# Performance work log

Measured on AMD Instinct MI355X. Metric: run time of the kernel, lower is better.

The kernel has to match this reference:

```python
import jax, jax.numpy as jnp
import numpy as np

N_NODES = 50000
N_EDGES = 800000
D_FEAT = 128
N_LAYERS = 3
HALF = 64  # units // 2 per kernel in tf_geometric MeanGraphSage
HIDDEN = 256
NUM_LABELS = 40


def setup_inputs() -> dict:
    key = jax.random.key(0)
    ks = jax.random.split(key, 6)
    x = jax.random.normal(ks[0], (N_NODES, D_FEAT), dtype=jnp.float32)
    edge_index = jax.random.randint(ks[1], (2, N_EDGES), 0, N_NODES, dtype=jnp.int32)
    self_kernels = jax.random.normal(ks[2], (N_LAYERS, D_FEAT, HALF), dtype=jnp.float32) * 0.05
    neighbor_kernels = jax.random.normal(ks[3], (N_LAYERS, D_FEAT, HALF), dtype=jnp.float32) * 0.05
    biases = jnp.zeros((N_LAYERS, 2 * HALF), dtype=jnp.float32)
    mlp_w1 = jax.random.normal(ks[4], (2 * HALF, HIDDEN), dtype=jnp.float32) * 0.05
    mlp_b1 = jnp.zeros((HIDDEN,), dtype=jnp.float32)
    mlp_w2 = jax.random.normal(ks[5], (HIDDEN, NUM_LABELS), dtype=jnp.float32) * 0.05
    mlp_b2 = jnp.zeros((NUM_LABELS,), dtype=jnp.float32)
    return {"x": x, "edge_index": edge_index, "self_kernels": self_kernels,
            "neighbor_kernels": neighbor_kernels, "biases": biases,
            "mlp_w1": mlp_w1, "mlp_b1": mlp_b1, "mlp_w2": mlp_w2, "mlp_b2": mlp_b2}


def reference(x, edge_index, self_kernels, neighbor_kernels, biases,
              mlp_w1, mlp_b1, mlp_w2, mlp_b2):
    n = x.shape[0]
    row, col = edge_index[0], edge_index[1]  # row: target node, col: source node
    # in-degree counts (graph is fixed across layers)
    ones = jnp.ones((edge_index.shape[1],), dtype=x.dtype)
    deg = jax.ops.segment_sum(ones, row, num_segments=n)  # [N]
    inv_deg = (1.0 / jnp.maximum(deg, 1.0))[:, None]      # [N,1]

    h = x
    for i in range(N_LAYERS):
        # mean-neighbor aggregation: gather source feats, segment-sum to targets
        nbr_sum = jax.ops.segment_sum(h[col], row, num_segments=n)  # [N,D]
        nbr_mean = nbr_sum * inv_deg
        from_self = h @ self_kernels[i]        # [N,HALF]
        from_nbr = nbr_mean @ neighbor_kernels[i]  # [N,HALF]
        h = jax.nn.relu(jnp.concatenate([from_self, from_nbr], axis=1) + biases[i])

    # MLP head (Flatten on [N,128] is a no-op)
    h = jax.nn.relu(h @ mlp_w1 + mlp_b1)
    return h @ mlp_w2 + mlp_b2
```

## Files before the change

kernel.cpp:

```cpp
#include <hip/hip_runtime.h>
#include <hip/hip_bf16.h>
#include <cstdint>
#include <cstddef>

#define N_NODES 50000
#define N_PAD   50176
#define N_EDGES 800000
#define D_FEAT  128
#define HALF    64
#define HIDDEN  256
#define LABELS  40

#define NBUCK 196
#define BCAP  5632
#define EDGES_PER_BLK 4096

#define HID_STRIDE 264

typedef __attribute__((ext_vector_type(8))) short bf16x8;
typedef __attribute__((ext_vector_type(4))) float f32x4;

#define PK_SELF(L) ((size_t)(L) * 8192)
#define PK_NBR(L)  (24576 + (size_t)(L) * 8192)
#define PK_W1      49152
#define PK_W2      81920
#define PK_TOTAL   94208

__device__ inline uint16_t f2bf_bits(float f) {
    __hip_bfloat16 b = __float2bfloat16(f);
    uint16_t u; __builtin_memcpy(&u, &b, 2); return u;
}

__global__ __launch_bounds__(1024) void bucket_scatter_kernel(
        const int* __restrict__ row, const int* __restrict__ col,
        int* __restrict__ bucket_cursor, uint32_t* __restrict__ staged) {
    __shared__ int hist[NBUCK];
    __shared__ int hbase[NBUCK];
    int tid  = threadIdx.x;
    int e0   = blockIdx.x * EDGES_PER_BLK;
    int eend = e0 + EDGES_PER_BLK; if (eend > N_EDGES) eend = N_EDGES;

    for (int i = tid; i < NBUCK; i += 1024) hist[i] = 0;
    __syncthreads();

    int rr[4], cc[4]; int ne = 0;
    for (int e = e0 + tid; e < eend; e += 1024) {
        rr[ne] = row[e]; cc[ne] = col[e]; ne++;
    }
    for (int i = 0; i < ne; i++) atomicAdd(&hist[rr[i] >> 8], 1);
    __syncthreads();

    for (int i = tid; i < NBUCK; i += 1024) {
        hbase[i] = atomicAdd(&bucket_cursor[i], hist[i]);
        hist[i]  = 0;
    }
    __syncthreads();

    for (int i = 0; i < ne; i++) {
        int b   = rr[i] >> 8;
        int off = atomicAdd(&hist[b], 1);
        int pos = hbase[b] + off;
        if (pos < BCAP)
            staged[(size_t)b * BCAP + pos] =
                ((uint32_t)(rr[i] & 255) << 16) | (uint32_t)cc[i];
    }
}

__global__ __launch_bounds__(1024) void bucket_fill_kernel(
        const uint32_t* __restrict__ staged, const int* __restrict__ bucket_cursor,
        int* __restrict__ deg, int* __restrict__ rowstart,
        float* __restrict__ inv_deg, int* __restrict__ csr_col) {
    __shared__ int cnt[256];
    __shared__ int excl[256];
    __shared__ int wt[4];
    __shared__ int seg[BCAP];
    __shared__ int base_s;
    int b   = blockIdx.x;
    int tid = threadIdx.x;

    if (tid < 64) {
        int partial = 0;
        for (int i = tid; i < b; i += 64) partial += bucket_cursor[i];
#pragma unroll
        for (int off = 32; off > 0; off >>= 1)
            partial += __shfl_down(partial, off, 64);
        if (tid == 0) base_s = partial;
    }
    if (tid < 256) cnt[tid] = 0;
    __syncthreads();

    int total = bucket_cursor[b]; if (total > BCAP) total = BCAP;
    int gbase = base_s;
    const uint32_t* st = staged + (size_t)b * BCAP;

    for (int i = tid; i < total; i += 1024) atomicAdd(&cnt[st[i] >> 16], 1);
    __syncthreads();

    int lane = tid & 63, wid = tid >> 6;
    int v = 0, s = 0;
    if (tid < 256) {
        v = cnt[tid]; s = v;
#pragma unroll
        for (int off = 1; off < 64; off <<= 1) {
            int t = __shfl_up(s, off, 64);
            if (lane >= off) s += t;
        }
        if (lane == 63) wt[wid] = s;
    }
    __syncthreads();
    if (tid == 0) { int a = 0; for (int i = 0; i < 4; i++) { int t = wt[i]; wt[i] = a; a += t; } }
    __syncthreads();
    if (tid < 256) {
        int ex = s - v + wt[wid];
        excl[tid] = ex;
        int node = (b << 8) + tid;
        if (node < N_NODES) {
            deg[node]      = v;
            rowstart[node] = gbase + ex;
            inv_deg[node]  = 1.0f / fmaxf((float)v, 1.0f);
        }
    }
    __syncthreads();
    for (int i = tid; i < total; i += 1024) {
        uint32_t u = st[i];
        int p = atomicAdd(&excl[u >> 16], 1);
        seg[p] = (int)(u & 0xffffu);
    }
    __syncthreads();
    for (int i = tid; i < total; i += 1024) csr_col[gbase + i] = seg[i];
}

__global__ __launch_bounds__(256) void xcast_kernel(
        const float* __restrict__ x, __hip_bfloat16* __restrict__ xb) {
    size_t i = (size_t)(blockIdx.x * blockDim.x + threadIdx.x) * 4;
    if (i >= (size_t)N_NODES * D_FEAT) return;
    float4 v = *(const float4*)(x + i);
    uint2 p;
    p.x = (uint32_t)f2bf_bits(v.x) | ((uint32_t)f2bf_bits(v.y) << 16);
    p.y = (uint32_t)f2bf_bits(v.z) | ((uint32_t)f2bf_bits(v.w) << 16);
    *(uint2*)((uint16_t*)xb + i) = p;
}

__global__ __launch_bounds__(256) void pack_all_kernel(
        const float* __restrict__ selfk, const float* __restrict__ nbrk,
        const float* __restrict__ w1, const float* __restrict__ w2,
        __hip_bfloat16* __restrict__ wpack) {
    int m = blockIdx.y;
    const float* W; int K, Ncols, Npad; size_t dstoff;
    if (m < 3)      { W = selfk + (size_t)m*D_FEAT*HALF;      K=128; Ncols=64;  Npad=64;  dstoff = PK_SELF(m); }
    else if (m < 6) { W = nbrk  + (size_t)(m-3)*D_FEAT*HALF;  K=128; Ncols=64;  Npad=64;  dstoff = PK_NBR(m-3); }
    else if (m == 6){ W = w1;                                 K=128; Ncols=256; Npad=256; dstoff = PK_W1; }
    else            { W = w2;                                 K=256; Ncols=40;  Npad=48;  dstoff = PK_W2; }
    int ksteps = K / 32;
    int total  = ksteps * (Npad / 16) * 64;
    int t = blockIdx.x * blockDim.x + threadIdx.x;
    if (t >= total) return;
    int lane = t & 63;
    int rest = t >> 6;
    int ks   = rest % ksteps;
    int ns   = rest / ksteps;
    int colb = ns * 16 + (lane & 15);
    int kb   = ks * 32 + (lane >> 4) * 8;
    __hip_bfloat16* dst = wpack + dstoff + (size_t)t * 8;
#pragma unroll
    for (int j = 0; j < 8; j++) {
        float v = (colb < Ncols) ? W[(size_t)(kb + j) * Ncols + colb] : 0.f;
        dst[j] = __float2bfloat16(v);
    }
}

__global__ __launch_bounds__(256) void agg4_kernel(
        const __hip_bfloat16* __restrict__ h, const int* __restrict__ csr_col,
        const int* __restrict__ rowstart, const int* __restrict__ deg,
        const float* __restrict__ inv_deg, __hip_bfloat16* __restrict__ nbr) {
    int gid  = blockIdx.x * blockDim.x + threadIdx.x;
    int wnum = gid >> 6;
    int lane = threadIdx.x & 63;
    int sub  = lane >> 4;
    int sl   = lane & 15;
    int node = wnum * 4 + sub;
    int start = rowstart[node];
    int d     = deg[node];
    const uint32_t* hw = (const uint32_t*)h;
    float acc[8] = {};

#define ACC8(U)                                        \
    acc[0] += __uint_as_float((U).x << 16);            \
    acc[1] += __uint_as_float((U).x & 0xffff0000u);    \
    acc[2] += __uint_as_float((U).y << 16);            \
    acc[3] += __uint_as_float((U).y & 0xffff0000u);    \
    acc[4] += __uint_as_float((U).z << 16);            \
    acc[5] += __uint_as_float((U).z & 0xffff0000u);    \
    acc[6] += __uint_as_float((U).w << 16);            \
    acc[7] += __uint_as_float((U).w & 0xffff0000u);

    if (d > 0) {
        int last = start + d - 1;
        int s[8];
#pragma unroll
        for (int k = 0; k < 8; k++) s[k] = csr_col[min(start + k, last)];
        int j = 0;
        for (; j + 8 <= d; j += 8) {
            int p[8];
#pragma unroll
            for (int k = 0; k < 8; k++) p[k] = csr_col[min(start + j + 8 + k, last)];
            uint4 u0 = *(const uint4*)(hw + (size_t)s[0] * 64 + sl * 4);
            uint4 u1 = *(const uint4*)(hw + (size_t)s[1] * 64 + sl * 4);
            uint4 u2 = *(const uint4*)(hw + (size_t)s[2] * 64 + sl * 4);
            uint4 u3 = *(const uint4*)(hw + (size_t)s[3] * 64 + sl * 4);
            uint4 u4 = *(const uint4*)(hw + (size_t)s[4] * 64 + sl * 4);
            uint4 u5 = *(const uint4*)(hw + (size_t)s[5] * 64 + sl * 4);
            uint4 u6 = *(const uint4*)(hw + (size_t)s[6] * 64 + sl * 4);
            uint4 u7 = *(const uint4*)(hw + (size_t)s[7] * 64 + sl * 4);
            ACC8(u0); ACC8(u1); ACC8(u2); ACC8(u3);
            ACC8(u4); ACC8(u5); ACC8(u6); ACC8(u7);
#pragma unroll
            for (int k = 0; k < 8; k++) s[k] = p[k];
        }
        int r = d - j;
#pragma unroll
        for (int k = 0; k < 8; k++) {
            if (k < r) {
                uint4 u = *(const uint4*)(hw + (size_t)s[k] * 64 + sl * 4);
                ACC8(u);
            }
        }
    }
#undef ACC8

    float inv = inv_deg[node];
    uint4 p;
    p.x = (uint32_t)f2bf_bits(acc[0] * inv) | ((uint32_t)f2bf_bits(acc[1] * inv) << 16);
    p.y = (uint32_t)f2bf_bits(acc[2] * inv) | ((uint32_t)f2bf_bits(acc[3] * inv) << 16);
    p.z = (uint32_t)f2bf_bits(acc[4] * inv) | ((uint32_t)f2bf_bits(acc[5] * inv) << 16);
    p.w = (uint32_t)f2bf_bits(acc[6] * inv) | ((uint32_t)f2bf_bits(acc[7] * inv) << 16);
    *(uint4*)((uint32_t*)nbr + (size_t)node * 64 + sl * 4) = p;
}

__global__ __launch_bounds__(256, 2) void layer_fused_kernel(
        const __hip_bfloat16* __restrict__ h, const __hip_bfloat16* __restrict__ nbr,
        const __hip_bfloat16* __restrict__ wpack_self,
        const __hip_bfloat16* __restrict__ wpack_nbr,
        const float* __restrict__ bias, __hip_bfloat16* __restrict__ out) {
    int wave = threadIdx.x >> 6, lane = threadIdx.x & 63;
    int row0 = blockIdx.x * 128 + wave * 32;
    int lrow = lane & 15, lgrp = lane >> 4;
    const __hip_bfloat16* hr0 = h   + (size_t)(row0 + lrow) * D_FEAT + lgrp * 8;
    const __hip_bfloat16* hr1 = hr0 + (size_t)16 * D_FEAT;
    const __hip_bfloat16* nr0 = nbr + (size_t)(row0 + lrow) * D_FEAT + lgrp * 8;
    const __hip_bfloat16* nr1 = nr0 + (size_t)16 * D_FEAT;

    f32x4 accS[2][4] = {};
    f32x4 accN[2][4] = {};
#pragma unroll
    for (int ks = 0; ks < 4; ks++) {
        bf16x8 ah0 = *(const bf16x8*)(hr0 + ks * 32);
        bf16x8 ah1 = *(const bf16x8*)(hr1 + ks * 32);
        bf16x8 an0 = *(const bf16x8*)(nr0 + ks * 32);
        bf16x8 an1 = *(const bf16x8*)(nr1 + ks * 32);
#pragma unroll
        for (int ns = 0; ns < 4; ns++) {
            bf16x8 bs = *(const bf16x8*)(wpack_self + ((size_t)(ns * 4 + ks) * 64 + lane) * 8);
            accS[0][ns] = __builtin_amdgcn_mfma_f32_16x16x32_bf16(ah0, bs, accS[0][ns], 0, 0, 0);
            accS[1][ns] = __builtin_amdgcn_mfma_f32_16x16x32_bf16(ah1, bs, accS[1][ns], 0, 0, 0);
            bf16x8 bn = *(const bf16x8*)(wpack_nbr + ((size_t)(ns * 4 + ks) * 64 + lane) * 8);
            accN[0][ns] = __builtin_amdgcn_mfma_f32_16x16x32_bf16(an0, bn, accN[0][ns], 0, 0, 0);
            accN[1][ns] = __builtin_amdgcn_mfma_f32_16x16x32_bf16(an1, bn, accN[1][ns], 0, 0, 0);
        }
    }
#pragma unroll
    for (int t = 0; t < 2; t++) {
#pragma unroll
        for (int ns = 0; ns < 4; ns++) {
            int colS = ns * 16 + lrow;
            int colN = HALF + colS;
            float bvS = bias[colS];
            float bvN = bias[colN];
#pragma unroll
            for (int i = 0; i < 4; i++) {
                int r = row0 + t * 16 + lgrp * 4 + i;
                out[(size_t)r * D_FEAT + colS] =
                    __float2bfloat16(fmaxf(accS[t][ns][i] + bvS, 0.f));
                out[(size_t)r * D_FEAT + colN] =
                    __float2bfloat16(fmaxf(accN[t][ns][i] + bvN, 0.f));
            }
        }
    }
}

__global__ __launch_bounds__(256, 2) void mlp_fused_kernel(
        const __hip_bfloat16* __restrict__ h, const __hip_bfloat16* __restrict__ w1p,
        const float* __restrict__ b1, const __hip_bfloat16* __restrict__ w2p,
        const float* __restrict__ b2, float* __restrict__ out) {
    __shared__ __align__(16) uint16_t hid[128 * HID_STRIDE];
    int wave = threadIdx.x >> 6, lane = threadIdx.x & 63;
    int row0 = blockIdx.x * 128 + wave * 32;
    int lrow = lane & 15, lgrp = lane >> 4;

    {
        const __hip_bfloat16* ar0 = h + (size_t)(row0 + lrow) * D_FEAT + lgrp * 8;
        const __hip_bfloat16* ar1 = ar0 + (size_t)16 * D_FEAT;
        f32x4 acc[2][16] = {};
#pragma unroll 1
        for (int ks = 0; ks < 4; ks++) {
            bf16x8 a0 = *(const bf16x8*)(ar0 + ks * 32);
            bf16x8 a1 = *(const bf16x8*)(ar1 + ks * 32);
#pragma unroll
            for (int ns = 0; ns < 16; ns++) {
                bf16x8 bfr = *(const bf16x8*)(w1p + ((size_t)(ns * 4 + ks) * 64 + lane) * 8);
                acc[0][ns] = __builtin_amdgcn_mfma_f32_16x16x32_bf16(a0, bfr, acc[0][ns], 0, 0, 0);
                acc[1][ns] = __builtin_amdgcn_mfma_f32_16x16x32_bf16(a1, bfr, acc[1][ns], 0, 0, 0);
            }
        }
        int lbase = wave * 32;
#pragma unroll
        for (int t = 0; t < 2; t++) {
#pragma unroll
            for (int ns = 0; ns < 16; ns++) {
                int col = ns * 16 + lrow;
                float bv = b1[col];
#pragma unroll
                for (int i = 0; i < 4; i++) {
                    int lr = lbase + t * 16 + lgrp * 4 + i;
                    hid[lr * HID_STRIDE + col] =
                        f2bf_bits(fmaxf(acc[t][ns][i] + bv, 0.f));
                }
            }
        }
    }
    __syncthreads();

    const uint16_t* br0 = &hid[(wave * 32 + lrow) * HID_STRIDE + lgrp * 8];
    const uint16_t* br1 = br0 + 16 * HID_STRIDE;
    f32x4 acc2[2][3] = {};
#pragma unroll
    for (int ks = 0; ks < 8; ks++) {
        bf16x8 a0 = *(const bf16x8*)(br0 + ks * 32);
        bf16x8 a1 = *(const bf16x8*)(br1 + ks * 32);
#pragma unroll
        for (int ns = 0; ns < 3; ns++) {
            bf16x8 bfr = *(const bf16x8*)(w2p + ((size_t)(ns * 8 + ks) * 64 + lane) * 8);
            acc2[0][ns] = __builtin_amdgcn_mfma_f32_16x16x32_bf16(a0, bfr, acc2[0][ns], 0, 0, 0);
            acc2[1][ns] = __builtin_amdgcn_mfma_f32_16x16x32_bf16(a1, bfr, acc2[1][ns], 0, 0, 0);
        }
    }
#pragma unroll
    for (int t = 0; t < 2; t++) {
#pragma unroll
        for (int ns = 0; ns < 3; ns++) {
            int col = ns * 16 + lrow;
            if (col < LABELS) {
                float bv = b2[col];
#pragma unroll
                for (int i = 0; i < 4; i++) {
                    int r = row0 + t * 16 + lgrp * 4 + i;
                    if (r < N_NODES)
                        out[(size_t)r * LABELS + col] = acc2[t][ns][i] + bv;
                }
            }
        }
    }
}

extern "C" void kernel_launch(void* const* d_in, const int* in_sizes, int n_in,
                              void* d_out, int out_size, void* d_ws, size_t ws_size,
                              hipStream_t stream) {
    const float* x      = (const float*)d_in[0];
    const int*   ei     = (const int*)d_in[1];
    const float* selfk  = (const float*)d_in[2];
    const float* nbrk   = (const float*)d_in[3];
    const float* biases = (const float*)d_in[4];
    const float* w1     = (const float*)d_in[5];
    const float* b1     = (const float*)d_in[6];
    const float* w2     = (const float*)d_in[7];
    const float* b2     = (const float*)d_in[8];
    float* out = (float*)d_out;

    const int* row = ei;
    const int* col = ei + N_EDGES;

    char* ws = (char*)d_ws;
    size_t off = 0;
    auto alloc = [&](size_t bytes) -> char* {
        char* p = ws + off;
        off = (off + bytes + 255) & ~(size_t)255;
        return p;
    };
    int*   deg       = (int*)  alloc((size_t)N_NODES * 4);
    int*   rowstart  = (int*)  alloc((size_t)N_NODES * 4);
    float* inv_deg   = (float*)alloc((size_t)N_NODES * 4);
    int*   bucket_cursor = (int*)alloc(256 * 4);
    int*   csr_col   = (int*)  alloc((size_t)N_EDGES * 4);
    uint32_t* staged = (uint32_t*)alloc((size_t)NBUCK * BCAP * 4);
    __hip_bfloat16* wpack  = (__hip_bfloat16*)alloc(PK_TOTAL * 2);
    __hip_bfloat16* xb     = (__hip_bfloat16*)alloc((size_t)N_PAD * D_FEAT * 2);
    __hip_bfloat16* hA     = (__hip_bfloat16*)alloc((size_t)N_PAD * D_FEAT * 2);
    __hip_bfloat16* hB     = (__hip_bfloat16*)alloc((size_t)N_PAD * D_FEAT * 2);
    __hip_bfloat16* nbrbuf = (__hip_bfloat16*)alloc((size_t)N_PAD * D_FEAT * 2);

    hipMemsetAsync(bucket_cursor, 0, 256 * 4, stream);

    const int scat_blocks = (N_EDGES + EDGES_PER_BLK - 1) / EDGES_PER_BLK;
    bucket_scatter_kernel<<<scat_blocks, 1024, 0, stream>>>(row, col, bucket_cursor, staged);
    bucket_fill_kernel<<<NBUCK, 1024, 0, stream>>>(staged, bucket_cursor,
                                                   deg, rowstart, inv_deg, csr_col);

    xcast_kernel<<<(N_NODES * D_FEAT / 4 + 255) / 256, 256, 0, stream>>>(x, xb);
    dim3 pgrid(16, 8);
    pack_all_kernel<<<pgrid, 256, 0, stream>>>(selfk, nbrk, w1, w2, wpack);

    const int agg_blocks   = N_NODES / 16;
    const int layer_blocks = N_PAD / 128;
    const int mlp_blocks   = N_PAD / 128;

    const __hip_bfloat16* hcur = xb;
    __hip_bfloat16* bufs[3] = {hA, hB, hA};
    for (int L = 0; L < 3; L++) {
        agg4_kernel<<<agg_blocks, 256, 0, stream>>>(hcur, csr_col, rowstart, deg,
                                                    inv_deg, nbrbuf);
        layer_fused_kernel<<<layer_blocks, 256, 0, stream>>>(
            hcur, nbrbuf, wpack + PK_SELF(L), wpack + PK_NBR(L),
            biases + (size_t)L * (2 * HALF), bufs[L]);
        hcur = bufs[L];
    }

    mlp_fused_kernel<<<mlp_blocks, 256, 0, stream>>>(hcur, wpack + PK_W1, b1,
                                                     wpack + PK_W2, b2, out);
}
```

Baseline: 247.4 us.

## Store node features in 16-column panels to localize gathers per panel

Reorganizes all bf16 feature buffers into 8 panels of 16 features each and splits the neighbor aggregation across panels, so each block gathers 32-byte slices from a single panel. This aims to keep the working set of the random gather small enough to stay cache-resident rather than streaming full 256-byte rows. The layer and MLP kernels are adapted to read and write the panel layout. The cost is re-reading the CSR indices and degree data once per panel and issuing more, smaller loads.

```diff
diff --git a/kernel.cpp b/kernel.cpp
--- a/kernel.cpp
+++ b/kernel.cpp
@@ -16,6 +16,8 @@
 #define EDGES_PER_BLK 4096
 
 #define HID_STRIDE 264
+
+#define PANE ((size_t)N_PAD * 16)
 
 typedef __attribute__((ext_vector_type(8))) short bf16x8;
 typedef __attribute__((ext_vector_type(4))) float f32x4;
@@ -130,15 +132,24 @@
     for (int i = tid; i < total; i += 1024) csr_col[gbase + i] = seg[i];
 }
 
-__global__ __launch_bounds__(256) void xcast_kernel(
-        const float* __restrict__ x, __hip_bfloat16* __restrict__ xb) {
-    size_t i = (size_t)(blockIdx.x * blockDim.x + threadIdx.x) * 4;
-    if (i >= (size_t)N_NODES * D_FEAT) return;
-    float4 v = *(const float4*)(x + i);
-    uint2 p;
-    p.x = (uint32_t)f2bf_bits(v.x) | ((uint32_t)f2bf_bits(v.y) << 16);
-    p.y = (uint32_t)f2bf_bits(v.z) | ((uint32_t)f2bf_bits(v.w) << 16);
-    *(uint2*)((uint16_t*)xb + i) = p;
+__global__ __launch_bounds__(256) void xcast_panel_kernel(
+        const float* __restrict__ x, __hip_bfloat16* __restrict__ hP) {
+    int idx = blockIdx.x * blockDim.x + threadIdx.x;
+    if (idx >= 8 * N_NODES * 2) return;
+    int p    = idx / (N_NODES * 2);
+    int rem  = idx - p * (N_NODES * 2);
+    int node = rem >> 1;
+    int half = rem & 1;
+    const float* src = x + (size_t)node * D_FEAT + p * 16 + half * 8;
+    float4 v0 = *(const float4*)src;
+    float4 v1 = *(const float4*)(src + 4);
+    uint2 o0, o1;
+    o0.x = (uint32_t)f2bf_bits(v0.x) | ((uint32_t)f2bf_bits(v0.y) << 16);
+    o0.y = (uint32_t)f2bf_bits(v0.z) | ((uint32_t)f2bf_bits(v0.w) << 16);
+    o1.x = (uint32_t)f2bf_bits(v1.x) | ((uint32_t)f2bf_bits(v1.y) << 16);
+    o1.y = (uint32_t)f2bf_bits(v1.z) | ((uint32_t)f2bf_bits(v1.w) << 16);
+    uint32_t* dst = (uint32_t*)(hP + (size_t)p * PANE + (size_t)node * 16 + half * 8);
+    dst[0] = o0.x; dst[1] = o0.y; dst[2] = o1.x; dst[3] = o1.y;
 }
 
 __global__ __launch_bounds__(256) void pack_all_kernel(
@@ -169,30 +180,28 @@
     }
 }
 
-__global__ __launch_bounds__(256) void agg4_kernel(
-        const __hip_bfloat16* __restrict__ h, const int* __restrict__ csr_col,
+__global__ __launch_bounds__(256) void agg_panel_kernel(
+        const __hip_bfloat16* __restrict__ hP, const int* __restrict__ csr_col,
         const int* __restrict__ rowstart, const int* __restrict__ deg,
-        const float* __restrict__ inv_deg, __hip_bfloat16* __restrict__ nbr) {
-    int gid  = blockIdx.x * blockDim.x + threadIdx.x;
-    int wnum = gid >> 6;
-    int lane = threadIdx.x & 63;
-    int sub  = lane >> 4;
-    int sl   = lane & 15;
-    int node = wnum * 4 + sub;
-    int start = rowstart[node];
-    int d     = deg[node];
-    const uint32_t* hw = (const uint32_t*)h;
-    float acc[8] = {};
-
-#define ACC8(U)                                        \
+        const float* __restrict__ inv_deg, __hip_bfloat16* __restrict__ nbrP) {
+    int panel = blockIdx.x & 7;
+    int chunk = blockIdx.x >> 3;
+    int wave  = threadIdx.x >> 6;
+    int lane  = threadIdx.x & 63;
+    int sub   = lane >> 2;
+    int q     = lane & 3;
+    int node  = (chunk * 4 + wave) * 16 + sub;
+    int ne    = min(node, N_NODES - 1);
+    int start = rowstart[ne];
+    int d     = deg[ne];
+    const uint32_t* hw = (const uint32_t*)(hP + (size_t)panel * PANE);
+    float acc[4] = {};
+
+#define ACC4(U)                                        \
     acc[0] += __uint_as_float((U).x << 16);            \
     acc[1] += __uint_as_float((U).x & 0xffff0000u);    \
     acc[2] += __uint_as_float((U).y << 16);            \
-    acc[3] += __uint_as_float((U).y & 0xffff0000u);    \
-    acc[4] += __uint_as_float((U).z << 16);            \
-    acc[5] += __uint_as_float((U).z & 0xffff0000u);    \
-    acc[6] += __uint_as_float((U).w << 16);            \
-    acc[7] += __uint_as_float((U).w & 0xffff0000u);
+    acc[3] += __uint_as_float((U).y & 0xffff0000u);
 
     if (d > 0) {
         int last = start + d - 1;
@@ -204,16 +213,16 @@
             int p[8];
 #pragma unroll
             for (int k = 0; k < 8; k++) p[k] = csr_col[min(start + j + 8 + k, last)];
-            uint4 u0 = *(const uint4*)(hw + (size_t)s[0] * 64 + sl * 4);
-            uint4 u1 = *(const uint4*)(hw + (size_t)s[1] * 64 + sl * 4);
-            uint4 u2 = *(const uint4*)(hw + (size_t)s[2] * 64 + sl * 4);
-            uint4 u3 = *(const uint4*)(hw + (size_t)s[3] * 64 + sl * 4);
-            uint4 u4 = *(const uint4*)(hw + (size_t)s[4] * 64 + sl * 4);
-            uint4 u5 = *(const uint4*)(hw + (size_t)s[5] * 64 + sl * 4);
-            uint4 u6 = *(const uint4*)(hw + (size_t)s[6] * 64 + sl * 4);
-            uint4 u7 = *(const uint4*)(hw + (size_t)s[7] * 64 + sl * 4);
-            ACC8(u0); ACC8(u1); ACC8(u2); ACC8(u3);
-            ACC8(u4); ACC8(u5); ACC8(u6); ACC8(u7);
+            uint2 u0 = *(const uint2*)(hw + (size_t)s[0] * 8 + q * 2);
+            uint2 u1 = *(const uint2*)(hw + (size_t)s[1] * 8 + q * 2);
+            uint2 u2 = *(const uint2*)(hw + (size_t)s[2] * 8 + q * 2);
+            uint2 u3 = *(const uint2*)(hw + (size_t)s[3] * 8 + q * 2);
+            uint2 u4 = *(const uint2*)(hw + (size_t)s[4] * 8 + q * 2);
+            uint2 u5 = *(const uint2*)(hw + (size_t)s[5] * 8 + q * 2);
+            uint2 u6 = *(const uint2*)(hw + (size_t)s[6] * 8 + q * 2);
+            uint2 u7 = *(const uint2*)(hw + (size_t)s[7] * 8 + q * 2);
+            ACC4(u0); ACC4(u1); ACC4(u2); ACC4(u3);
+            ACC4(u4); ACC4(u5); ACC4(u6); ACC4(u7);
 #pragma unroll
             for (int k = 0; k < 8; k++) s[k] = p[k];
         }
@@ -221,20 +230,18 @@
 #pragma unroll
         for (int k = 0; k < 8; k++) {
             if (k < r) {
-                uint4 u = *(const uint4*)(hw + (size_t)s[k] * 64 + sl * 4);
-                ACC8(u);
+                uint2 u = *(const uint2*)(hw + (size_t)s[k] * 8 + q * 2);
+                ACC4(u);
             }
         }
     }
-#undef ACC8
-
-    float inv = inv_deg[node];
-    uint4 p;
+#undef ACC4
+
+    float inv = inv_deg[ne];
+    uint2 p;
     p.x = (uint32_t)f2bf_bits(acc[0] * inv) | ((uint32_t)f2bf_bits(acc[1] * inv) << 16);
     p.y = (uint32_t)f2bf_bits(acc[2] * inv) | ((uint32_t)f2bf_bits(acc[3] * inv) << 16);
-    p.z = (uint32_t)f2bf_bits(acc[4] * inv) | ((uint32_t)f2bf_bits(acc[5] * inv) << 16);
-    p.w = (uint32_t)f2bf_bits(acc[6] * inv) | ((uint32_t)f2bf_bits(acc[7] * inv) << 16);
-    *(uint4*)((uint32_t*)nbr + (size_t)node * 64 + sl * 4) = p;
+    *(uint2*)((uint32_t*)(nbrP + (size_t)panel * PANE) + (size_t)node * 8 + q * 2) = p;
 }
 
 __global__ __launch_bounds__(256, 2) void layer_fused_kernel(
@@ -245,19 +252,19 @@
     int wave = threadIdx.x >> 6, lane = threadIdx.x & 63;
     int row0 = blockIdx.x * 128 + wave * 32;
     int lrow = lane & 15, lgrp = lane >> 4;
-    const __hip_bfloat16* hr0 = h   + (size_t)(row0 + lrow) * D_FEAT + lgrp * 8;
-    const __hip_bfloat16* hr1 = hr0 + (size_t)16 * D_FEAT;
-    const __hip_bfloat16* nr0 = nbr + (size_t)(row0 + lrow) * D_FEAT + lgrp * 8;
-    const __hip_bfloat16* nr1 = nr0 + (size_t)16 * D_FEAT;
+    size_t psel = (size_t)(lgrp >> 1) * PANE;
+    size_t rb0  = (size_t)(row0 + lrow) * 16 + (lgrp & 1) * 8;
+    size_t rb1  = rb0 + 16 * 16;
 
     f32x4 accS[2][4] = {};
     f32x4 accN[2][4] = {};
 #pragma unroll
     for (int ks = 0; ks < 4; ks++) {
-        bf16x8 ah0 = *(const bf16x8*)(hr0 + ks * 32);
-        bf16x8 ah1 = *(const bf16x8*)(hr1 + ks * 32);
-        bf16x8 an0 = *(const bf16x8*)(nr0 + ks * 32);
-        bf16x8 an1 = *(const bf16x8*)(nr1 + ks * 32);
+        size_t pk = psel + (size_t)(ks * 2) * PANE;
+        bf16x8 ah0 = *(const bf16x8*)(h   + pk + rb0);
+        bf16x8 ah1 = *(const bf16x8*)(h   + pk + rb1);
+        bf16x8 an0 = *(const bf16x8*)(nbr + pk + rb0);
+        bf16x8 an1 = *(const bf16x8*)(nbr + pk + rb1);
 #pragma unroll
         for (int ns = 0; ns < 4; ns++) {
             bf16x8 bs = *(const bf16x8*)(wpack_self + ((size_t)(ns * 4 + ks) * 64 + lane) * 8);
@@ -272,16 +279,14 @@
     for (int t = 0; t < 2; t++) {
 #pragma unroll
         for (int ns = 0; ns < 4; ns++) {
-            int colS = ns * 16 + lrow;
-            int colN = HALF + colS;
-            float bvS = bias[colS];
-            float bvN = bias[colN];
+            float bvS = bias[ns * 16 + lrow];
+            float bvN = bias[HALF + ns * 16 + lrow];
 #pragma unroll
             for (int i = 0; i < 4; i++) {
                 int r = row0 + t * 16 + lgrp * 4 + i;
-                out[(size_t)r * D_FEAT + colS] =
+                out[(size_t)ns * PANE + (size_t)r * 16 + lrow] =
                     __float2bfloat16(fmaxf(accS[t][ns][i] + bvS, 0.f));
-                out[(size_t)r * D_FEAT + colN] =
+                out[(size_t)(4 + ns) * PANE + (size_t)r * 16 + lrow] =
                     __float2bfloat16(fmaxf(accN[t][ns][i] + bvN, 0.f));
             }
         }
@@ -298,13 +303,15 @@
     int lrow = lane & 15, lgrp = lane >> 4;
 
     {
-        const __hip_bfloat16* ar0 = h + (size_t)(row0 + lrow) * D_FEAT + lgrp * 8;
-        const __hip_bfloat16* ar1 = ar0 + (size_t)16 * D_FEAT;
+        size_t psel = (size_t)(lgrp >> 1) * PANE;
+        size_t rb0  = (size_t)(row0 + lrow) * 16 + (lgrp & 1) * 8;
+        size_t rb1  = rb0 + 16 * 16;
         f32x4 acc[2][16] = {};
 #pragma unroll 1
         for (int ks = 0; ks < 4; ks++) {
-            bf16x8 a0 = *(const bf16x8*)(ar0 + ks * 32);
-            bf16x8 a1 = *(const bf16x8*)(ar1 + ks * 32);
+            size_t pk = psel + (size_t)(ks * 2) * PANE;
+            bf16x8 a0 = *(const bf16x8*)(h + pk + rb0);
+            bf16x8 a1 = *(const bf16x8*)(h + pk + rb1);
 #pragma unroll
             for (int ns = 0; ns < 16; ns++) {
                 bf16x8 bfr = *(const bf16x8*)(w1p + ((size_t)(ns * 4 + ks) * 64 + lane) * 8);
@@ -405,19 +412,19 @@
     bucket_fill_kernel<<<NBUCK, 1024, 0, stream>>>(staged, bucket_cursor,
                                                    deg, rowstart, inv_deg, csr_col);
 
-    xcast_kernel<<<(N_NODES * D_FEAT / 4 + 255) / 256, 256, 0, stream>>>(x, xb);
+    xcast_panel_kernel<<<(8 * N_NODES * 2 + 255) / 256, 256, 0, stream>>>(x, xb);
     dim3 pgrid(16, 8);
     pack_all_kernel<<<pgrid, 256, 0, stream>>>(selfk, nbrk, w1, w2, wpack);
 
-    const int agg_blocks   = N_NODES / 16;
+    const int agg_blocks   = (N_PAD / 64) * 8;
     const int layer_blocks = N_PAD / 128;
     const int mlp_blocks   = N_PAD / 128;
 
     const __hip_bfloat16* hcur = xb;
     __hip_bfloat16* bufs[3] = {hA, hB, hA};
     for (int L = 0; L < 3; L++) {
-        agg4_kernel<<<agg_blocks, 256, 0, stream>>>(hcur, csr_col, rowstart, deg,
-                                                    inv_deg, nbrbuf);
+        agg_panel_kernel<<<agg_blocks, 256, 0, stream>>>(hcur, csr_col, rowstart, deg,
+                                                         inv_deg, nbrbuf);
         layer_fused_kernel<<<layer_blocks, 256, 0, stream>>>(
             hcur, nbrbuf, wpack + PK_SELF(L), wpack + PK_NBR(L),
             biases + (size_t)L * (2 * HALF), bufs[L]);
```

New measurement: 280.1 us. 13.2% more time.
